# Optimization experiments

Measured on AMD Instinct MI355X. Metric: run time of the kernel, lower is better.

## Reference

```python
import jax, jax.numpy as jnp
import numpy as np

N_AUTHOR, N_SUBJECT, N_PAPER = 200000, 50000, 100000
E = 1000000
D = 64
NEG_SLOPE = 0.01


def setup_inputs() -> dict:
    key = jax.random.key(0)
    ks = jax.random.split(key, 16)
    return {
        "feat_author": jax.random.normal(ks[0], (N_AUTHOR, D), jnp.float32),
        "feat_subject": jax.random.normal(ks[1], (N_SUBJECT, D), jnp.float32),
        "feat_paper": jax.random.normal(ks[2], (N_PAPER, D), jnp.float32),
        "edge_src_ap": jax.random.randint(ks[3], (E,), 0, N_AUTHOR, jnp.int32),
        "edge_dst_ap": jax.random.randint(ks[4], (E,), 0, N_PAPER, jnp.int32),
        "edge_src_sp": jax.random.randint(ks[5], (E,), 0, N_SUBJECT, jnp.int32),
        "edge_dst_sp": jax.random.randint(ks[6], (E,), 0, N_PAPER, jnp.int32),
        "attn_l_ap": jax.random.normal(ks[7], (D,), jnp.float32) * 0.1,
        "attn_r_ap": jax.random.normal(ks[8], (D,), jnp.float32) * 0.1,
        "attn_l_sp": jax.random.normal(ks[9], (D,), jnp.float32) * 0.1,
        "attn_r_sp": jax.random.normal(ks[10], (D,), jnp.float32) * 0.1,
        "fc_w": jax.random.normal(ks[11], (D, D), jnp.float32) * 0.1,
        "fc_b": jax.random.normal(ks[12], (D,), jnp.float32) * 0.1,
        "sem_attn": jax.random.normal(ks[13], (D,), jnp.float32) * 0.1,
    }


def heco_gat(feat_src, feat_dst, attn_l, attn_r, src, dst, n_dst):
    # per-node attention logits
    el = feat_src @ attn_l          # [Ns]
    er = feat_dst @ attn_r          # [Nd]
    e = el[src] + er[dst]           # [E]
    e = jnp.where(e > 0, e, NEG_SLOPE * e)  # leaky_relu
    # edge softmax grouped by destination node (numerically stable)
    emax = jax.ops.segment_max(e, dst, num_segments=n_dst)
    ee = jnp.exp(e - emax[dst])
    denom = jax.ops.segment_sum(ee, dst, num_segments=n_dst)
    a = ee / denom[dst]             # [E]
    # weighted scatter-sum aggregation
    out = jax.ops.segment_sum(a[:, None] * feat_src[src], dst, num_segments=n_dst)
    return jax.nn.elu(out)


def semantic_attention(h, fc_w, fc_b, sem_attn):
    # h: [N, M, d]
    w = jnp.tanh(h @ fc_w.T + fc_b).mean(axis=0) @ sem_attn  # [M]
    beta = jax.nn.softmax(w)                                  # [M]
    return jnp.einsum("m,nmd->nd", beta, h)


def reference(feat_author, feat_subject, feat_paper,
              edge_src_ap, edge_dst_ap, edge_src_sp, edge_dst_sp,
              attn_l_ap, attn_r_ap, attn_l_sp, attn_r_sp,
              fc_w, fc_b, sem_attn):
    n_dst = feat_paper.shape[0]
    h_ap = heco_gat(feat_author, feat_paper, attn_l_ap, attn_r_ap,
                    edge_src_ap, edge_dst_ap, n_dst)
    h_sp = heco_gat(feat_subject, feat_paper, attn_l_sp, attn_r_sp,
                    edge_src_sp, edge_dst_sp, n_dst)
    h = jnp.stack([h_ap, h_sp], axis=1)  # [N_dst, 2, D]
    return semantic_attention(h, fc_w, fc_b, sem_attn)
```

## Files before the change

kernel.cpp:

```cpp
#include <hip/hip_runtime.h>
#include <math.h>

#define N_AUTHOR 200000
#define N_SUBJECT 50000
#define N_PAPER 100000
#define NEDGE 1000000
#define D 64
#define NEG_SLOPE 0.01f

#define NSLOT (2 * N_PAPER)
#define CHUNK 1024
#define NCHUNK ((NSLOT + CHUNK - 1) / CHUNK)
#define DROWS (N_AUTHOR + N_SUBJECT + N_PAPER)

__device__ __forceinline__ float bcast(float v, int lane) {
    return __uint_as_float((unsigned)__builtin_amdgcn_readlane(__float_as_int(v), lane));
}
__device__ __forceinline__ int bcast_i(int v, int lane) {
    return __builtin_amdgcn_readlane(v, lane);
}
__device__ __forceinline__ float fast_tanh(float x) {
    x = fminf(15.0f, fmaxf(-15.0f, x));
    float ex = __expf(2.0f * x);
    return (ex - 1.0f) / (ex + 1.0f);
}


__global__ void dots_hist_kernel(const float* __restrict__ fa,
                                 const float* __restrict__ fs,
                                 const float* __restrict__ fp,
                                 const float* __restrict__ al_ap,
                                 const float* __restrict__ ar_ap,
                                 const float* __restrict__ al_sp,
                                 const float* __restrict__ ar_sp,
                                 float* __restrict__ el_ap,
                                 float* __restrict__ el_sp,
                                 float* __restrict__ er_ap,
                                 float* __restrict__ er_sp,
                                 const int* __restrict__ dst_ap,
                                 const int* __restrict__ dst_sp,
                                 int* __restrict__ count,
                                 int nb_dots) {
    if ((int)blockIdx.x < nb_dots) {
        int row  = blockIdx.x * 4 + (threadIdx.x >> 6);
        int lane = threadIdx.x & 63;
        if (row < N_AUTHOR) {
            float v = fa[(size_t)row * D + lane] * al_ap[lane];
#pragma unroll
            for (int o = 32; o > 0; o >>= 1) v += __shfl_xor(v, o, 64);
            if (lane == 0) el_ap[row] = v;
        } else if (row < N_AUTHOR + N_SUBJECT) {
            int r = row - N_AUTHOR;
            float v = fs[(size_t)r * D + lane] * al_sp[lane];
#pragma unroll
            for (int o = 32; o > 0; o >>= 1) v += __shfl_xor(v, o, 64);
            if (lane == 0) el_sp[r] = v;
        } else if (row < DROWS) {
            int r = row - (N_AUTHOR + N_SUBJECT);
            float f  = fp[(size_t)r * D + lane];
            float v0 = f * ar_ap[lane];
            float v1 = f * ar_sp[lane];
#pragma unroll
            for (int o = 32; o > 0; o >>= 1) {
                v0 += __shfl_xor(v0, o, 64);
                v1 += __shfl_xor(v1, o, 64);
            }
            if (lane == 0) { er_ap[r] = v0; er_sp[r] = v1; }
        }
    } else {
        int i = (blockIdx.x - nb_dots) * blockDim.x + threadIdx.x;
        if (i < NEDGE)          atomicAdd(&count[dst_ap[i]], 1);
        else if (i < 2 * NEDGE) atomicAdd(&count[N_PAPER + dst_sp[i - NEDGE]], 1);
    }
}

__global__ void chunk_sum_kernel(const int* __restrict__ count, int* __restrict__ psum) {
    __shared__ int red[4];
    int base = blockIdx.x * CHUNK;
    int t = threadIdx.x;
    int s = 0;
#pragma unroll
    for (int j = 0; j < 4; ++j) {
        int idx = base + t * 4 + j;
        if (idx < NSLOT) s += count[idx];
    }
#pragma unroll
    for (int o = 32; o > 0; o >>= 1) s += __shfl_xor(s, o, 64);
    if ((t & 63) == 0) red[t >> 6] = s;
    __syncthreads();
    if (t == 0) psum[blockIdx.x] = red[0] + red[1] + red[2] + red[3];
}

__global__ void scan_partials_kernel(int* __restrict__ psum) {
    __shared__ int buf[256];
    int t = threadIdx.x;
    buf[t] = (t < NCHUNK) ? psum[t] : 0;
    __syncthreads();
    for (int off = 1; off < 256; off <<= 1) {
        int v = (t >= off) ? buf[t - off] : 0;
        __syncthreads();
        buf[t] += v;
        __syncthreads();
    }
    if (t < NCHUNK) psum[t] = t ? buf[t - 1] : 0;
}

__global__ void chunk_scan_kernel(const int* __restrict__ count,
                                  const int* __restrict__ psum,
                                  int* __restrict__ row_ptr,
                                  int* __restrict__ cursor) {
    __shared__ int ts[256];
    int base = blockIdx.x * CHUNK;
    int t = threadIdx.x;
    int loc[4];
    int s = 0;
#pragma unroll
    for (int j = 0; j < 4; ++j) {
        int idx = base + t * 4 + j;
        loc[j] = (idx < NSLOT) ? count[idx] : 0;
        s += loc[j];
    }
    ts[t] = s;
    __syncthreads();
    for (int off = 1; off < 256; off <<= 1) {
        int v = (t >= off) ? ts[t - off] : 0;
        __syncthreads();
        ts[t] += v;
        __syncthreads();
    }
    int ex = (t ? ts[t - 1] : 0) + psum[blockIdx.x];
#pragma unroll
    for (int j = 0; j < 4; ++j) {
        int idx = base + t * 4 + j;
        if (idx < NSLOT) {
            row_ptr[idx] = ex;
            cursor[idx]  = ex;
            ex += loc[j];
        }
    }
    if (blockIdx.x == 0 && t == 0) row_ptr[NSLOT] = 2 * NEDGE;
}

__global__ void scatter2_kernel(const int* __restrict__ src_ap,
                                const int* __restrict__ dst_ap,
                                const int* __restrict__ src_sp,
                                const int* __restrict__ dst_sp,
                                const float* __restrict__ el_ap,
                                const float* __restrict__ er_ap,
                                const float* __restrict__ el_sp,
                                const float* __restrict__ er_sp,
                                int* __restrict__ cursor,
                                int2* __restrict__ rec) {
    const int nthreads = 2 * NEDGE / 4;
    int tid = blockIdx.x * blockDim.x + threadIdx.x;
    if (tid >= nthreads) return;
#pragma unroll
    for (int k = 0; k < 4; ++k) {
        int i = tid + k * nthreads;
        int s, dslot; float e;
        if (i < NEDGE) {
            s = src_ap[i];
            int d = dst_ap[i];
            e = el_ap[s] + er_ap[d];
            dslot = d;
        } else {
            int j = i - NEDGE;
            s = src_sp[j];
            int d = dst_sp[j];
            e = el_sp[s] + er_sp[d];
            dslot = N_PAPER + d;
        }
        e = e > 0.0f ? e : NEG_SLOPE * e;
        int pos = atomicAdd(&cursor[dslot], 1);
        rec[pos] = make_int2(s, __float_as_int(e));
    }
}

__global__ void __launch_bounds__(256, 4)
node_gat_fused_kernel(const int* __restrict__ row_ptr,
                      const int2* __restrict__ rec,
                      const float* __restrict__ feat_author,
                      const float* __restrict__ feat_subject,
                      float* __restrict__ h_ap,
                      float* __restrict__ h_sp,
                      const float* __restrict__ fc_w,
                      const float* __restrict__ fc_b,
                      const float* __restrict__ sem_attn,
                      float* __restrict__ wsum) {
    __shared__ float red[8];
    int wid  = threadIdx.x >> 6;
    int lane = threadIdx.x & 63;

    float fw[D];
    {
        const float4* fw4 = (const float4*)(fc_w + (size_t)lane * D);
#pragma unroll
        for (int k = 0; k < 16; ++k) {
            float4 v = fw4[k];
            fw[4 * k + 0] = v.x; fw[4 * k + 1] = v.y;
            fw[4 * k + 2] = v.z; fw[4 * k + 3] = v.w;
        }
    }
    float fb = fc_b[lane];
    float sa = sem_attn[lane];
    float tacc0 = 0.0f, tacc1 = 0.0f;

    for (int slot = blockIdx.x * 4 + wid; slot < NSLOT; slot += gridDim.x * 4) {
        int mp = slot >= N_PAPER;
        const float* feat = mp ? feat_subject : feat_author;
        int start = row_ptr[slot], end = row_ptr[slot + 1];
        int len = end - start;

        float hpre;
        if (len == 0) {
            hpre = 0.0f;
        } else if (len <= 64) {
            int2 r = make_int2(0, 0xff800000);
            if (lane < len) r = rec[start + lane];
            float ev = __int_as_float(r.y);
            float m = ev;
#pragma unroll
            for (int o = 32; o > 0; o >>= 1) m = fmaxf(m, __shfl_xor(m, o, 64));
            float w = (lane < len) ? __expf(ev - m) : 0.0f;
            float sden = w;
#pragma unroll
            for (int o = 32; o > 0; o >>= 1) sden += __shfl_xor(sden, o, 64);

            float a0 = 0.0f, a1 = 0.0f, a2 = 0.0f, a3 = 0.0f;
            int j = 0;
            for (; j + 4 <= len; j += 4) {
                float w0 = bcast(w, j),     w1 = bcast(w, j + 1);
                float w2 = bcast(w, j + 2), w3 = bcast(w, j + 3);
                int   s0 = bcast_i(r.x, j),     s1 = bcast_i(r.x, j + 1);
                int   s2 = bcast_i(r.x, j + 2), s3 = bcast_i(r.x, j + 3);
                a0 = fmaf(w0, feat[(size_t)s0 * D + lane], a0);
                a1 = fmaf(w1, feat[(size_t)s1 * D + lane], a1);
                a2 = fmaf(w2, feat[(size_t)s2 * D + lane], a2);
                a3 = fmaf(w3, feat[(size_t)s3 * D + lane], a3);
            }
            for (; j < len; ++j) {
                float w0 = bcast(w, j);
                int   s0 = bcast_i(r.x, j);
                a0 = fmaf(w0, feat[(size_t)s0 * D + lane], a0);
            }
            hpre = ((a0 + a1) + (a2 + a3)) / sden;
        } else {
            float m = -1e30f;
            for (int i = start + lane; i < end; i += 64)
                m = fmaxf(m, __int_as_float(rec[i].y));
#pragma unroll
            for (int o = 32; o > 0; o >>= 1) m = fmaxf(m, __shfl_xor(m, o, 64));
            float sdenl = 0.0f, accA = 0.0f, accB = 0.0f;
            for (int c = start; c < end; c += 64) {
                int rem = end - c; if (rem > 64) rem = 64;
                float wreg = 0.0f; int sreg = 0;
                if (lane < rem) {
                    int2 r = rec[c + lane];
                    wreg = __expf(__int_as_float(r.y) - m);
                    sreg = r.x;
                    sdenl += wreg;
                }
                int j = 0;
                for (; j + 2 <= rem; j += 2) {
                    float w0 = bcast(wreg, j), w1 = bcast(wreg, j + 1);
                    int   s0 = bcast_i(sreg, j), s1 = bcast_i(sreg, j + 1);
                    accA = fmaf(w0, feat[(size_t)s0 * D + lane], accA);
                    accB = fmaf(w1, feat[(size_t)s1 * D + lane], accB);
                }
                if (j < rem) {
                    float w0 = bcast(wreg, j);
                    int   s0 = bcast_i(sreg, j);
                    accA = fmaf(w0, feat[(size_t)s0 * D + lane], accA);
                }
            }
            float sden = sdenl;
#pragma unroll
            for (int o = 32; o > 0; o >>= 1) sden += __shfl_xor(sden, o, 64);
            hpre = (accA + accB) / sden;
        }

        float hv = hpre > 0.0f ? hpre : (__expf(hpre) - 1.0f);

        float* h = mp ? (h_sp + (size_t)(slot - N_PAPER) * D)
                      : (h_ap + (size_t)slot * D);
        h[lane] = hv;

        float acc2 = fb;
#pragma unroll
        for (int dd = 0; dd < D; ++dd)
            acc2 = fmaf(bcast(hv, dd), fw[dd], acc2);
        float t = fast_tanh(acc2) * sa;
#pragma unroll
        for (int o = 32; o > 0; o >>= 1) t += __shfl_xor(t, o, 64);
        if (mp) tacc1 += t; else tacc0 += t;
    }

    if (lane == 0) { red[wid] = tacc0; red[4 + wid] = tacc1; }
    __syncthreads();
    if (threadIdx.x == 0) atomicAdd(&wsum[0], red[0] + red[1] + red[2] + red[3]);
    if (threadIdx.x == 1) atomicAdd(&wsum[1], red[4] + red[5] + red[6] + red[7]);
}

__global__ void final_combine_kernel(float4* __restrict__ out,
                                     const float4* __restrict__ h_sp,
                                     const float* __restrict__ wsum,
                                     int n_vec4) {
    int i = blockIdx.x * blockDim.x + threadIdx.x;
    if (i >= n_vec4) return;
    float w0 = wsum[0] * (1.0f / N_PAPER);
    float w1 = wsum[1] * (1.0f / N_PAPER);
    float mx = fmaxf(w0, w1);
    float e0 = __expf(w0 - mx), e1 = __expf(w1 - mx);
    float inv = 1.0f / (e0 + e1);
    float b0 = e0 * inv, b1 = e1 * inv;
    float4 a = out[i], b = h_sp[i];
    out[i] = make_float4(b0 * a.x + b1 * b.x, b0 * a.y + b1 * b.y,
                         b0 * a.z + b1 * b.z, b0 * a.w + b1 * b.w);
}


extern "C" void kernel_launch(void* const* d_in, const int* in_sizes, int n_in,
                              void* d_out, int out_size, void* d_ws, size_t ws_size,
                              hipStream_t stream) {
    const float* feat_author = (const float*)d_in[0];
    const float* feat_subject= (const float*)d_in[1];
    const float* feat_paper  = (const float*)d_in[2];
    const int*   src_ap      = (const int*)d_in[3];
    const int*   dst_ap      = (const int*)d_in[4];
    const int*   src_sp      = (const int*)d_in[5];
    const int*   dst_sp      = (const int*)d_in[6];
    const float* attn_l_ap   = (const float*)d_in[7];
    const float* attn_r_ap   = (const float*)d_in[8];
    const float* attn_l_sp   = (const float*)d_in[9];
    const float* attn_r_sp   = (const float*)d_in[10];
    const float* fc_w        = (const float*)d_in[11];
    const float* fc_b        = (const float*)d_in[12];
    const float* sem_attn    = (const float*)d_in[13];

    float* out = (float*)d_out;

    char* ws = (char*)d_ws;
    size_t off = 0;
    auto alloc = [&](size_t bytes) {
        size_t r = off;
        off = (off + bytes + 255) & ~(size_t)255;
        return r;
    };
    int*   count   = (int*)(ws + alloc((size_t)NSLOT * 4));
    float* wsum    = (float*)(ws + alloc(2 * 4));
    size_t zero_bytes = off;
    int*   row_ptr = (int*)(ws + alloc((size_t)(NSLOT + 1) * 4));
    int*   cursor  = (int*)(ws + alloc((size_t)NSLOT * 4));
    int*   psum    = (int*)(ws + alloc((size_t)NCHUNK * 4));
    float* el_ap   = (float*)(ws + alloc((size_t)N_AUTHOR * 4));
    float* er_ap   = (float*)(ws + alloc((size_t)N_PAPER * 4));
    float* el_sp   = (float*)(ws + alloc((size_t)N_SUBJECT * 4));
    float* er_sp   = (float*)(ws + alloc((size_t)N_PAPER * 4));
    int2*  rec     = (int2*)(ws + alloc((size_t)(2 * NEDGE) * 8));
    float* h_sp    = (float*)(ws + alloc((size_t)N_PAPER * D * 4));
    (void)ws_size; (void)in_sizes; (void)n_in;

    hipMemsetAsync(d_ws, 0, zero_bytes, stream);

    const int B = 256;

    int nb_dots = (DROWS + 3) / 4;
    int nb_hist = (2 * NEDGE + B - 1) / B;
    dots_hist_kernel<<<nb_dots + nb_hist, B, 0, stream>>>(
        feat_author, feat_subject, feat_paper,
        attn_l_ap, attn_r_ap, attn_l_sp, attn_r_sp,
        el_ap, el_sp, er_ap, er_sp,
        dst_ap, dst_sp, count, nb_dots);

    chunk_sum_kernel<<<NCHUNK, B, 0, stream>>>(count, psum);
    scan_partials_kernel<<<1, 256, 0, stream>>>(psum);
    chunk_scan_kernel<<<NCHUNK, B, 0, stream>>>(count, psum, row_ptr, cursor);
    int s2grid = (2 * NEDGE / 4 + B - 1) / B;
    scatter2_kernel<<<s2grid, B, 0, stream>>>(src_ap, dst_ap, src_sp, dst_sp,
                                              el_ap, er_ap, el_sp, er_sp,
                                              cursor, rec);

    node_gat_fused_kernel<<<2048, B, 0, stream>>>(row_ptr, rec,
                                                  feat_author, feat_subject,
                                                  out, h_sp,
                                                  fc_w, fc_b, sem_attn, wsum);

    int n_vec4 = N_PAPER * D / 4;
    final_combine_kernel<<<(n_vec4 + B - 1) / B, B, 0, stream>>>(
        (float4*)out, (const float4*)h_sp, wsum, n_vec4);
}
```

Before: 581.8 us.

## Process two destination slots per wavefront and defer tanh reduction

Each wavefront now handles two adjacent destination slots at once, interleaving their softmax reductions, gathers and FC matvec. The goal is more independent memory loads in flight and better latency hiding for the gather-bound aggregation. The per-slot cross-lane reduction of the tanh term is moved out of the loop and done once per lane at the end. The costs are higher register pressure, possibly lower occupancy, and divergence when the two slots have different degrees.

```diff
diff --git a/kernel.cpp b/kernel.cpp
--- a/kernel.cpp
+++ b/kernel.cpp
@@ -203,99 +203,140 @@
     }
     float fb = fc_b[lane];
     float sa = sem_attn[lane];
-    float tacc0 = 0.0f, tacc1 = 0.0f;
-
-    for (int slot = blockIdx.x * 4 + wid; slot < NSLOT; slot += gridDim.x * 4) {
-        int mp = slot >= N_PAPER;
-        const float* feat = mp ? feat_subject : feat_author;
-        int start = row_ptr[slot], end = row_ptr[slot + 1];
-        int len = end - start;
-
-        float hpre;
-        if (len == 0) {
-            hpre = 0.0f;
-        } else if (len <= 64) {
-            int2 r = make_int2(0, 0xff800000);
-            if (lane < len) r = rec[start + lane];
-            float ev = __int_as_float(r.y);
-            float m = ev;
-#pragma unroll
-            for (int o = 32; o > 0; o >>= 1) m = fmaxf(m, __shfl_xor(m, o, 64));
-            float w = (lane < len) ? __expf(ev - m) : 0.0f;
-            float sden = w;
-#pragma unroll
-            for (int o = 32; o > 0; o >>= 1) sden += __shfl_xor(sden, o, 64);
-
-            float a0 = 0.0f, a1 = 0.0f, a2 = 0.0f, a3 = 0.0f;
-            int j = 0;
-            for (; j + 4 <= len; j += 4) {
-                float w0 = bcast(w, j),     w1 = bcast(w, j + 1);
-                float w2 = bcast(w, j + 2), w3 = bcast(w, j + 3);
-                int   s0 = bcast_i(r.x, j),     s1 = bcast_i(r.x, j + 1);
-                int   s2 = bcast_i(r.x, j + 2), s3 = bcast_i(r.x, j + 3);
-                a0 = fmaf(w0, feat[(size_t)s0 * D + lane], a0);
-                a1 = fmaf(w1, feat[(size_t)s1 * D + lane], a1);
-                a2 = fmaf(w2, feat[(size_t)s2 * D + lane], a2);
-                a3 = fmaf(w3, feat[(size_t)s3 * D + lane], a3);
+    float taccL0 = 0.0f, taccL1 = 0.0f;
+
+    for (int sA = blockIdx.x * 8 + wid * 2; sA < NSLOT; sA += gridDim.x * 8) {
+        int sB = sA + 1;
+        int startA = row_ptr[sA], endA = row_ptr[sA + 1];
+        int startB = endA,        endB = row_ptr[sB + 1];
+        int lenA = endA - startA, lenB = endB - startB;
+
+        float hvA, hvB;
+        if (lenA <= 64 && lenB <= 64) {
+            int2 rA = make_int2(0, 0xff800000);
+            int2 rB = make_int2(0, 0xff800000);
+            if (lane < lenA) rA = rec[startA + lane];
+            if (lane < lenB) rB = rec[startB + lane];
+            float evA = __int_as_float(rA.y), evB = __int_as_float(rB.y);
+            float mA = evA, mB = evB;
+#pragma unroll
+            for (int o = 32; o > 0; o >>= 1) {
+                mA = fmaxf(mA, __shfl_xor(mA, o, 64));
+                mB = fmaxf(mB, __shfl_xor(mB, o, 64));
             }
-            for (; j < len; ++j) {
-                float w0 = bcast(w, j);
-                int   s0 = bcast_i(r.x, j);
-                a0 = fmaf(w0, feat[(size_t)s0 * D + lane], a0);
+            float wA = (lane < lenA) ? __expf(evA - mA) : 0.0f;
+            float wB = (lane < lenB) ? __expf(evB - mB) : 0.0f;
+            float dA = wA, dB = wB;
+#pragma unroll
+            for (int o = 32; o > 0; o >>= 1) {
+                dA += __shfl_xor(dA, o, 64);
+                dB += __shfl_xor(dB, o, 64);
             }
-            hpre = ((a0 + a1) + (a2 + a3)) / sden;
-        } else {
-            float m = -1e30f;
-            for (int i = start + lane; i < end; i += 64)
-                m = fmaxf(m, __int_as_float(rec[i].y));
-#pragma unroll
-            for (int o = 32; o > 0; o >>= 1) m = fmaxf(m, __shfl_xor(m, o, 64));
-            float sdenl = 0.0f, accA = 0.0f, accB = 0.0f;
-            for (int c = start; c < end; c += 64) {
-                int rem = end - c; if (rem > 64) rem = 64;
-                float wreg = 0.0f; int sreg = 0;
-                if (lane < rem) {
-                    int2 r = rec[c + lane];
-                    wreg = __expf(__int_as_float(r.y) - m);
-                    sreg = r.x;
-                    sdenl += wreg;
+
+            const float* featA = (sA >= N_PAPER) ? feat_subject : feat_author;
+            const float* featB = (sB >= N_PAPER) ? feat_subject : feat_author;
+            float aA0 = 0.0f, aA1 = 0.0f, aB0 = 0.0f, aB1 = 0.0f;
+            int lenM = lenA > lenB ? lenA : lenB;
+            for (int j = 0; j < lenM; j += 2) {
+                if (j < lenA) {
+                    float w0 = bcast(wA, j); int s0 = bcast_i(rA.x, j);
+                    aA0 = fmaf(w0, featA[(size_t)s0 * D + lane], aA0);
+                    if (j + 1 < lenA) {
+                        float w1 = bcast(wA, j + 1); int s1 = bcast_i(rA.x, j + 1);
+                        aA1 = fmaf(w1, featA[(size_t)s1 * D + lane], aA1);
+                    }
                 }
-                int j = 0;
-                for (; j + 2 <= rem; j += 2) {
-                    float w0 = bcast(wreg, j), w1 = bcast(wreg, j + 1);
-                    int   s0 = bcast_i(sreg, j), s1 = bcast_i(sreg, j + 1);
-                    accA = fmaf(w0, feat[(size_t)s0 * D + lane], accA);
-                    accB = fmaf(w1, feat[(size_t)s1 * D + lane], accB);
-                }
-                if (j < rem) {
-                    float w0 = bcast(wreg, j);
-                    int   s0 = bcast_i(sreg, j);
-                    accA = fmaf(w0, feat[(size_t)s0 * D + lane], accA);
+                if (j < lenB) {
+                    float w0 = bcast(wB, j); int s0 = bcast_i(rB.x, j);
+                    aB0 = fmaf(w0, featB[(size_t)s0 * D + lane], aB0);
+                    if (j + 1 < lenB) {
+                        float w1 = bcast(wB, j + 1); int s1 = bcast_i(rB.x, j + 1);
+                        aB1 = fmaf(w1, featB[(size_t)s1 * D + lane], aB1);
+                    }
                 }
             }
-            float sden = sdenl;
-#pragma unroll
-            for (int o = 32; o > 0; o >>= 1) sden += __shfl_xor(sden, o, 64);
-            hpre = (accA + accB) / sden;
-        }
-
-        float hv = hpre > 0.0f ? hpre : (__expf(hpre) - 1.0f);
-
-        float* h = mp ? (h_sp + (size_t)(slot - N_PAPER) * D)
-                      : (h_ap + (size_t)slot * D);
-        h[lane] = hv;
-
-        float acc2 = fb;
-#pragma unroll
-        for (int dd = 0; dd < D; ++dd)
-            acc2 = fmaf(bcast(hv, dd), fw[dd], acc2);
-        float t = fast_tanh(acc2) * sa;
-#pragma unroll
-        for (int o = 32; o > 0; o >>= 1) t += __shfl_xor(t, o, 64);
-        if (mp) tacc1 += t; else tacc0 += t;
-    }
-
-    if (lane == 0) { red[wid] = tacc0; red[4 + wid] = tacc1; }
+            float hpreA = lenA ? (aA0 + aA1) / dA : 0.0f;
+            float hpreB = lenB ? (aB0 + aB1) / dB : 0.0f;
+            hvA = hpreA > 0.0f ? hpreA : (__expf(hpreA) - 1.0f);
+            hvB = hpreB > 0.0f ? hpreB : (__expf(hpreB) - 1.0f);
+        } else {
+            float hv2[2];
+#pragma unroll
+            for (int q = 0; q < 2; ++q) {
+                int st = q ? startB : startA, en = q ? endB : endA;
+                int sl = q ? sB : sA;
+                const float* feat = (sl >= N_PAPER) ? feat_subject : feat_author;
+                float m = -1e30f;
+                for (int i = st + lane; i < en; i += 64)
+                    m = fmaxf(m, __int_as_float(rec[i].y));
+#pragma unroll
+                for (int o = 32; o > 0; o >>= 1) m = fmaxf(m, __shfl_xor(m, o, 64));
+                float sdenl = 0.0f, accA = 0.0f, accB = 0.0f;
+                for (int c = st; c < en; c += 64) {
+                    int rem = en - c; if (rem > 64) rem = 64;
+                    float wreg = 0.0f; int sreg = 0;
+                    if (lane < rem) {
+                        int2 r = rec[c + lane];
+                        wreg = __expf(__int_as_float(r.y) - m);
+                        sreg = r.x;
+                        sdenl += wreg;
+                    }
+                    int j = 0;
+                    for (; j + 2 <= rem; j += 2) {
+                        float w0 = bcast(wreg, j), w1 = bcast(wreg, j + 1);
+                        int   s0 = bcast_i(sreg, j), s1 = bcast_i(sreg, j + 1);
+                        accA = fmaf(w0, feat[(size_t)s0 * D + lane], accA);
+                        accB = fmaf(w1, feat[(size_t)s1 * D + lane], accB);
+                    }
+                    if (j < rem) {
+                        float w0 = bcast(wreg, j);
+                        int   s0 = bcast_i(sreg, j);
+                        accA = fmaf(w0, feat[(size_t)s0 * D + lane], accA);
+                    }
+                }
+                float sden = sdenl;
+#pragma unroll
+                for (int o = 32; o > 0; o >>= 1) sden += __shfl_xor(sden, o, 64);
+                float hpre = (en > st) ? (accA + accB) / sden : 0.0f;
+                hv2[q] = hpre > 0.0f ? hpre : (__expf(hpre) - 1.0f);
+            }
+            hvA = hv2[0]; hvB = hv2[1];
+        }
+
+        float* hA = (sA >= N_PAPER) ? (h_sp + (size_t)(sA - N_PAPER) * D)
+                                    : (h_ap + (size_t)sA * D);
+        float* hB = (sB >= N_PAPER) ? (h_sp + (size_t)(sB - N_PAPER) * D)
+                                    : (h_ap + (size_t)sB * D);
+        hA[lane] = hvA;
+        hB[lane] = hvB;
+
+        float mA0 = 0.0f, mA1 = 0.0f, mA2 = 0.0f, mA3 = 0.0f;
+        float mB0 = 0.0f, mB1 = 0.0f, mB2 = 0.0f, mB3 = 0.0f;
+#pragma unroll
+        for (int dd = 0; dd < D; dd += 4) {
+            mA0 = fmaf(bcast(hvA, dd),     fw[dd],     mA0);
+            mB0 = fmaf(bcast(hvB, dd),     fw[dd],     mB0);
+            mA1 = fmaf(bcast(hvA, dd + 1), fw[dd + 1], mA1);
+            mB1 = fmaf(bcast(hvB, dd + 1), fw[dd + 1], mB1);
+            mA2 = fmaf(bcast(hvA, dd + 2), fw[dd + 2], mA2);
+            mB2 = fmaf(bcast(hvB, dd + 2), fw[dd + 2], mB2);
+            mA3 = fmaf(bcast(hvA, dd + 3), fw[dd + 3], mA3);
+            mB3 = fmaf(bcast(hvB, dd + 3), fw[dd + 3], mB3);
+        }
+        float yA = fb + ((mA0 + mA1) + (mA2 + mA3));
+        float yB = fb + ((mB0 + mB1) + (mB2 + mB3));
+        float tA = fast_tanh(yA) * sa;
+        float tB = fast_tanh(yB) * sa;
+        if (sA >= N_PAPER) taccL1 += tA; else taccL0 += tA;
+        if (sB >= N_PAPER) taccL1 += tB; else taccL0 += tB;
+    }
+
+#pragma unroll
+    for (int o = 32; o > 0; o >>= 1) {
+        taccL0 += __shfl_xor(taccL0, o, 64);
+        taccL1 += __shfl_xor(taccL1, o, 64);
+    }
+    if (lane == 0) { red[wid] = taccL0; red[4 + wid] = taccL1; }
     __syncthreads();
     if (threadIdx.x == 0) atomicAdd(&wsum[0], red[0] + red[1] + red[2] + red[3]);
     if (threadIdx.x == 1) atomicAdd(&wsum[1], red[4] + red[5] + red[6] + red[7]);
```

Result: no change. 590.6 us (+1.5%).
